# Optimization experiments

Hardware: AMD Instinct MI355X
Metric: run time of the kernel (lower is better)

Reference implementation:

```python
import jax, jax.numpy as jnp
import numpy as np

# Poincare ball with curvature c = 1.0 (geoopt conventions)
C = 1.0
SQC = 1.0  # sqrt(c)
ATANH_EPS = 1e-5
MAXNORM = (1.0 - 4e-3) / SQC  # geoopt float32 projx boundary eps = 4e-3
HD = 256  # hyperbolic_dim


def _norm(x):
    return jnp.clip(jnp.linalg.norm(x, axis=-1, keepdims=True), 1e-15)


def _artanh(x):
    return jnp.arctanh(jnp.clip(x, -1.0 + ATANH_EPS, 1.0 - ATANH_EPS))


def expmap0(u):
    n = _norm(u)
    return jnp.tanh(SQC * n) * u / (SQC * n)


def logmap0(y):
    n = _norm(y)
    return _artanh(SQC * n) * y / (SQC * n)


def projx(x):
    n = _norm(x)
    return jnp.where(n > MAXNORM, x * (MAXNORM / n), x)


def mobius_add(x, y):
    x2 = jnp.sum(x * x, -1, keepdims=True)
    y2 = jnp.sum(y * y, -1, keepdims=True)
    xy = jnp.sum(x * y, -1, keepdims=True)
    num = (1.0 + 2.0 * C * xy + C * y2) * x + (1.0 - C * x2) * y
    den = 1.0 + 2.0 * C * xy + C * C * x2 * y2
    return num / jnp.clip(den, 1e-15)


def mobius_matvec(x, W):
    # geoopt mobius_matvec(weight.T, x) == hyperbolic version of x @ W, W: (in, out)
    xn = _norm(x)
    mx = x @ W
    mxn = _norm(mx)
    return jnp.tanh((mxn / xn) * _artanh(SQC * xn)) * mx / (SQC * mxn)


def mobius_scalar_mul(r, x):
    n = _norm(x)
    return jnp.tanh(r * _artanh(SQC * n)) * x / (SQC * n)


def hlinear(x, W, b):
    # HyperbolicLinear.forward (geoopt manifold ops project by default)
    return projx(mobius_add(projx(mobius_matvec(x, W)), b))


def mobius_tanh(x):
    # MobiusTanh.forward
    return projx(expmap0(jnp.tanh(logmap0(x))))


def zscore(x, eps=1e-8):
    m = jnp.mean(x, axis=1, keepdims=True)
    s = jnp.std(x, axis=1, keepdims=True, ddof=1)  # torch.std is unbiased
    return (x - m) / (s + eps)


def _make_params(key):
    dims_d = [(1711, 1024), (1024, 512), (512, HD)]
    dims_t = [(1711, 1024), (1024, 512), (512, HD)]
    dims_m = [(HD, 64), (64, 32), (32, 2)]
    params = {}
    names = [('Wd', dims_d), ('Wt', dims_t), ('Wm', dims_m)]
    k = key
    for prefix, dims in names:
        for i, (fi, fo) in enumerate(dims, start=1):
            k, k1, k2 = jax.random.split(k, 3)
            params[f'{prefix}{i}'] = jax.random.normal(k1, (fi, fo), dtype=jnp.float32)
            bt = jax.random.normal(k2, (fo,), dtype=jnp.float32) * 0.01
            params[f'b{prefix[1]}{i}'] = expmap0(bt)
    return params


def setup_inputs() -> dict:
    key = jax.random.key(0)
    ks = jax.random.split(key, 8)
    B = 16384
    inp = {
        'drug_chembert': jax.random.normal(ks[0], (B, 768), dtype=jnp.float32),
        'drug_pc': jax.random.normal(ks[1], (B, 11), dtype=jnp.float32),
        'drug_maccs': jax.random.normal(ks[2], (B, 167), dtype=jnp.float32),
        'drug_ecfp': jax.random.normal(ks[3], (B, 765), dtype=jnp.float32),
        'target_esm': jax.random.normal(ks[4], (B, 1280), dtype=jnp.float32),
        'target_pc': jax.random.normal(ks[5], (B, 11), dtype=jnp.float32),
        'target_mer': jax.random.normal(ks[6], (B, 420), dtype=jnp.float32),
    }
    inp.update(_make_params(ks[7]))
    return inp


def reference(drug_chembert, drug_pc, drug_maccs, drug_ecfp,
              target_esm, target_pc, target_mer,
              Wd1, bd1, Wd2, bd2, Wd3, bd3,
              Wt1, bt1, Wt2, bt2, Wt3, bt3,
              Wm1, bm1, Wm2, bm2, Wm3, bm3):
    drug = jnp.concatenate([zscore(drug_chembert), zscore(drug_pc),
                            zscore(drug_maccs), zscore(drug_ecfp)], axis=1)  # [B,1711]
    targ = jnp.concatenate([zscore(target_esm), zscore(target_pc),
                            zscore(target_mer)], axis=1)  # [B,1711]

    h = mobius_tanh(hlinear(expmap0(drug), Wd1, bd1))
    h = mobius_tanh(hlinear(h, Wd2, bd2))
    head = hlinear(h, Wd3, bd3)  # [B,HD]

    t = mobius_tanh(hlinear(expmap0(targ), Wt1, bt1))
    t = mobius_tanh(hlinear(t, Wt2, bt2))
    tail = hlinear(t, Wt3, bt3)  # [B,HD]

    mid = projx(mobius_add(mobius_scalar_mul(0.27, head),
                           mobius_scalar_mul(0.73, tail)))

    r = mobius_tanh(hlinear(mid, Wm1, bm1))
    r = mobius_tanh(hlinear(r, Wm2, bm2))
    return hlinear(r, Wm3, bm3)  # [B,2]
```

## Files before the change

### kernel.cpp

```cpp
#include <hip/hip_runtime.h>
#include <math.h>

#define MAXNORM_F 0.996f

typedef __attribute__((ext_vector_type(8))) short bf16x8;
typedef __attribute__((ext_vector_type(4))) float f32x4;

__device__ __forceinline__ short f2bf(float f) {
    union { float f; unsigned u; } v; v.f = f;
    unsigned r = v.u + 0x7FFF + ((v.u >> 16) & 1);
    return (short)(r >> 16);
}
__device__ __forceinline__ float bf2f(short s) {
    union { unsigned u; float f; } v; v.u = ((unsigned)(unsigned short)s) << 16;
    return v.f;
}

__device__ __forceinline__ float artanh_c(float x) {
    const float lim = 1.0f - 1e-5f;
    x = fminf(fmaxf(x, -lim), lim);
    return 0.5f * logf((1.0f + x) / (1.0f - x));
}

__device__ __forceinline__ float wsum(float v) {
#pragma unroll
    for (int m = 32; m > 0; m >>= 1) v += __shfl_xor(v, m, 64);
    return v;
}

__global__ __launch_bounds__(256) void pack_w_kernel(
    const float* __restrict__ W, int Kreal, int KB, int N, short* __restrict__ out) {
    int e = blockIdx.x * 256 + threadIdx.x;
    int total = (N >> 7) * KB * 2 * 4096;
    if (e >= total) return;
    int j   = e & 7;
    int n   = (e >> 3) & 127;
    int kg  = (e >> 10) & 3;
    int seg = (e >> 12) & 1;
    int rest = e >> 13;
    int kb  = rest % KB;
    int nt  = rest / KB;
    int k = (kb << 5) + (kg << 3) + j;
    int col = (nt << 7) + n;
    float v = (k < Kreal) ? W[(size_t)k * N + col] : 0.f;
    short hi = f2bf(v);
    out[e] = (seg == 0) ? hi : f2bf(v - bf2f(hi));
}

__global__ __launch_bounds__(256) void prep_kernel(
    const float* __restrict__ s0, const float* __restrict__ s1,
    const float* __restrict__ s2, const float* __restrict__ s3,
    int f0, int f1, int f2, int f3,
    short* __restrict__ Xb, float* __restrict__ xn_out) {
    __shared__ float xbuf[4][1712];
    const int lane = threadIdx.x & 63, wave = threadIdx.x >> 6;
    const int row = blockIdx.x * 4 + wave;
    float* xb = xbuf[wave];
    const float* srcs[4] = {s0, s1, s2, s3};
    const int fs[4] = {f0, f1, f2, f3};
    int off = 0;
    for (int b = 0; b < 4; b++) {
        int F = fs[b];
        if (F == 0) break;
        const float* srow = srcs[b] + (size_t)row * F;
        float ps = 0.f;
        for (int i = lane; i < F; i += 64) { float v = srow[i]; xb[off + i] = v; ps += v; }
        float mean = wsum(ps) / (float)F;
        float pq = 0.f;
        for (int i = lane; i < F; i += 64) { float d = xb[off + i] - mean; pq += d * d; }
        float var = wsum(pq) / (float)(F - 1);
        float inv = 1.0f / (sqrtf(var) + 1e-8f);
        for (int i = lane; i < F; i += 64) xb[off + i] = (xb[off + i] - mean) * inv;
        off += F;
    }
    float pn = 0.f;
    for (int i = lane; i < 1711; i += 64) pn += xb[i] * xb[i];
    float n = fmaxf(sqrtf(wsum(pn)), 1e-15f);
    float t = tanhf(n);
    float sc = t / n;
    short* xrow = Xb + (size_t)row * 3456;
    for (int i = lane; i < 1728; i += 64) {
        float v = (i < 1711) ? sc * xb[i] : 0.f;
        short hi = f2bf(v);
        int base = (i >> 5) * 64 + (i & 31);
        xrow[base] = hi;
        xrow[base + 32] = f2bf(v - bf2f(hi));
    }
    if (lane == 0) xn_out[row] = fmaxf(t, 1e-15f);
}

__global__ __launch_bounds__(256) void gemm_mfma(
    const short* __restrict__ A, int lda, int KB,
    const short* __restrict__ Wp,
    float* __restrict__ C, int N, int ntShift) {
    __shared__ short As[2][8192];
    __shared__ short Bs[2][8192];
    const int tid = threadIdx.x;
    const int lane = tid & 63;
    const int wave = __builtin_amdgcn_readfirstlane(tid >> 6);
    const int waveM = wave >> 1, waveN = wave & 1;
    const int kg = lane >> 4, l16 = lane & 15;

    int flat = blockIdx.x;
    int xcd = flat & 7;
    int idx = flat >> 3;
    int q = idx >> ntShift;
    int nt = idx & ((1 << ntShift) - 1);
    int mt = q * 8 + xcd;
    const int m0 = mt * 128;

    f32x4 acc[4][4] = {};
    const short* Bbase = Wp + (size_t)nt * KB * 8192;

    auto stage = [&](int b, int kb) {
#pragma unroll
        for (int c = 0; c < 4; c++) {
            int u = c * 256 + wave * 64 + lane;
            int row = u >> 3;
            int p = (u & 7) ^ (row & 7);
            const short* ga = A + (size_t)(m0 + row) * lda + kb * 64 + p * 8;
            __builtin_amdgcn_global_load_lds(
                (const __attribute__((address_space(1))) unsigned int*)ga,
                (__attribute__((address_space(3))) unsigned int*)&As[b][(c * 256 + wave * 64) * 8],
                16, 0, 0);
        }
#pragma unroll
        for (int c = 0; c < 4; c++) {
            int u = c * 256 + wave * 64 + lane;
            const short* gb = Bbase + (size_t)kb * 8192 + u * 8;
            __builtin_amdgcn_global_load_lds(
                (const __attribute__((address_space(1))) unsigned int*)gb,
                (__attribute__((address_space(3))) unsigned int*)&Bs[b][(c * 256 + wave * 64) * 8],
                16, 0, 0);
        }
    };

    stage(0, 0);
    __syncthreads();
    int cur = 0;
    for (int kb = 0; kb < KB; kb++) {
        if (kb + 1 < KB) stage(cur ^ 1, kb + 1);
        bf16x8 ah[4], al[4], bh[4], bl[4];
#pragma unroll
        for (int mi = 0; mi < 4; mi++) {
            int r = waveM * 64 + mi * 16 + l16;
            int uh = r * 8 + (kg ^ (r & 7));
            int ul = r * 8 + ((4 + kg) ^ (r & 7));
            ah[mi] = *(const bf16x8*)&As[cur][uh * 8];
            al[mi] = *(const bf16x8*)&As[cur][ul * 8];
        }
#pragma unroll
        for (int ni = 0; ni < 4; ni++) {
            int n = waveN * 64 + ni * 16 + l16;
            bh[ni] = *(const bf16x8*)&Bs[cur][(kg * 128 + n) * 8];
            bl[ni] = *(const bf16x8*)&Bs[cur][(512 + kg * 128 + n) * 8];
        }
        __builtin_amdgcn_s_setprio(1);
#pragma unroll
        for (int mi = 0; mi < 4; mi++)
#pragma unroll
            for (int ni = 0; ni < 4; ni++)
                acc[mi][ni] = __builtin_amdgcn_mfma_f32_16x16x32_bf16(ah[mi], bh[ni], acc[mi][ni], 0, 0, 0);
#pragma unroll
        for (int mi = 0; mi < 4; mi++)
#pragma unroll
            for (int ni = 0; ni < 4; ni++)
                acc[mi][ni] = __builtin_amdgcn_mfma_f32_16x16x32_bf16(al[mi], bh[ni], acc[mi][ni], 0, 0, 0);
#pragma unroll
        for (int mi = 0; mi < 4; mi++)
#pragma unroll
            for (int ni = 0; ni < 4; ni++)
                acc[mi][ni] = __builtin_amdgcn_mfma_f32_16x16x32_bf16(ah[mi], bl[ni], acc[mi][ni], 0, 0, 0);
        __builtin_amdgcn_s_setprio(0);
        __syncthreads();
        cur ^= 1;
    }
    const int rbase = m0 + waveM * 64 + (lane >> 4) * 4;
    const int cbase = nt * 128 + waveN * 64 + l16;
#pragma unroll
    for (int mi = 0; mi < 4; mi++)
#pragma unroll
        for (int ni = 0; ni < 4; ni++)
#pragma unroll
            for (int r = 0; r < 4; r++)
                C[(size_t)(rbase + mi * 16 + r) * N + cbase + ni * 16] = acc[mi][ni][r];
}

template<int E>
__device__ float hyper_head_w(float (&v)[E], const float (&bv)[E], float xn, int do_tanh) {
    float p = 0.f;
#pragma unroll
    for (int e = 0; e < E; e++) p += v[e] * v[e];
    float mxn = fmaxf(sqrtf(wsum(p)), 1e-15f);
    float t1 = tanhf((mxn / xn) * artanh_c(xn));
    float ny = fmaxf(t1, 1e-15f);
    float fac = (ny > MAXNORM_F) ? (MAXNORM_F / ny) : 1.0f;
    float sm = t1 * fac / mxn;
    float pa2 = 0.f, pab = 0.f, pb2 = 0.f;
#pragma unroll
    for (int e = 0; e < E; e++) {
        v[e] *= sm;
        pa2 += v[e] * v[e]; pab += v[e] * bv[e]; pb2 += bv[e] * bv[e];
    }
    float a2 = wsum(pa2);
    float ab = wsum(pab);
    float b2 = wsum(pb2);
    float den = fmaxf(1.0f + 2.0f * ab + a2 * b2, 1e-15f);
    float ca = (1.0f + 2.0f * ab + b2) / den;
    float cb = (1.0f - a2) / den;
    float pz2 = 0.f;
#pragma unroll
    for (int e = 0; e < E; e++) {
        v[e] = ca * v[e] + cb * bv[e];
        pz2 += v[e] * v[e];
    }
    float nz = fmaxf(sqrtf(wsum(pz2)), 1e-15f);
    float fz = (nz > MAXNORM_F) ? (MAXNORM_F / nz) : 1.0f;
    float nzp = nz * fz;
    if (!do_tanh) {
#pragma unroll
        for (int e = 0; e < E; e++) v[e] *= fz;
        return nzp;
    }
    float ia = artanh_c(nzp) / nzp * fz;
    float pt2 = 0.f;
#pragma unroll
    for (int e = 0; e < E; e++) {
        v[e] = tanhf(ia * v[e]);
        pt2 += v[e] * v[e];
    }
    float ntn = fmaxf(sqrtf(wsum(pt2)), 1e-15f);
    float to = tanhf(ntn);
    float no = fmaxf(to, 1e-15f);
    float fo = (no > MAXNORM_F) ? (MAXNORM_F / no) : 1.0f;
    float so = to / ntn * fo;
#pragma unroll
    for (int e = 0; e < E; e++) v[e] *= so;
    return fminf(no, MAXNORM_F);
}

template<int VPT>
__global__ __launch_bounds__(256) void epi_kernel(
    const float* __restrict__ MX, int N, const float* __restrict__ bias,
    float* __restrict__ xn_io, short* __restrict__ Xout, int ldx,
    float* __restrict__ Fout, int do_tanh) {
    const int lane = threadIdx.x & 63, wave = threadIdx.x >> 6;
    const int row = blockIdx.x * 4 + wave;
    const float* mrow = MX + (size_t)row * N;
    float v[4 * VPT], bv[4 * VPT];
#pragma unroll
    for (int j = 0; j < VPT; j++) {
        int idx = j * 256 + lane * 4;
        float4 t = *(const float4*)(mrow + idx);
        v[4 * j] = t.x; v[4 * j + 1] = t.y; v[4 * j + 2] = t.z; v[4 * j + 3] = t.w;
        float4 tb = *(const float4*)(bias + idx);
        bv[4 * j] = tb.x; bv[4 * j + 1] = tb.y; bv[4 * j + 2] = tb.z; bv[4 * j + 3] = tb.w;
    }
    float xn = xn_io[row];
    float nrm = hyper_head_w<4 * VPT>(v, bv, xn, do_tanh);
    if (Xout) {
        short* orow = Xout + (size_t)row * ldx;
#pragma unroll
        for (int j = 0; j < VPT; j++) {
            int idx = j * 256 + lane * 4;
            int base = (idx >> 5) * 64 + (idx & 31);
            short4 h4, l4;
            short hi;
            hi = f2bf(v[4 * j + 0]); h4.x = hi; l4.x = f2bf(v[4 * j + 0] - bf2f(hi));
            hi = f2bf(v[4 * j + 1]); h4.y = hi; l4.y = f2bf(v[4 * j + 1] - bf2f(hi));
            hi = f2bf(v[4 * j + 2]); h4.z = hi; l4.z = f2bf(v[4 * j + 2] - bf2f(hi));
            hi = f2bf(v[4 * j + 3]); h4.w = hi; l4.w = f2bf(v[4 * j + 3] - bf2f(hi));
            *(short4*)(orow + base) = h4;
            *(short4*)(orow + base + 32) = l4;
        }
    }
    if (Fout) {
        float* orow = Fout + (size_t)row * N;
#pragma unroll
        for (int j = 0; j < VPT; j++) {
            int idx = j * 256 + lane * 4;
            float4 t;
            t.x = v[4 * j]; t.y = v[4 * j + 1]; t.z = v[4 * j + 2]; t.w = v[4 * j + 3];
            *(float4*)(orow + idx) = t;
        }
    }
    if (lane == 0) xn_io[row] = fmaxf(nrm, 1e-15f);
}

__global__ __launch_bounds__(256) void merge_mlp_kernel(
    const float* __restrict__ head, const float* __restrict__ tail,
    const float* __restrict__ nh_arr, const float* __restrict__ nt_arr,
    const float* __restrict__ Wm1, const float* __restrict__ bm1,
    const float* __restrict__ Wm2, const float* __restrict__ bm2,
    const float* __restrict__ Wm3, const float* __restrict__ bm3,
    float* __restrict__ out) {
    __shared__ float xs[4][256];
    const int lane = threadIdx.x & 63, wave = threadIdx.x >> 6;
    const int row = blockIdx.x * 4 + wave;
    float* x = xs[wave];
    float4 h4 = *(const float4*)(head + (size_t)row * 256 + lane * 4);
    float4 t4 = *(const float4*)(tail + (size_t)row * 256 + lane * 4);
    float A[4] = {h4.x, h4.y, h4.z, h4.w};
    float Bv[4] = {t4.x, t4.y, t4.z, t4.w};
    float nh = nh_arr[row], ntl = nt_arr[row];
    float sh = tanhf(0.27f * artanh_c(nh)) / nh;
    float st = tanhf(0.73f * artanh_c(ntl)) / ntl;
    float px2 = 0.f, py2 = 0.f, pxy = 0.f;
#pragma unroll
    for (int e = 0; e < 4; e++) {
        A[e] *= sh; Bv[e] *= st;
        px2 += A[e] * A[e]; py2 += Bv[e] * Bv[e]; pxy += A[e] * Bv[e];
    }
    float x2 = wsum(px2), y2 = wsum(py2), xy = wsum(pxy);
    float den = fmaxf(1.0f + 2.0f * xy + x2 * y2, 1e-15f);
    float ca = (1.0f + 2.0f * xy + y2) / den, cb = (1.0f - x2) / den;
    float z[4]; float pz2 = 0.f;
#pragma unroll
    for (int e = 0; e < 4; e++) { z[e] = ca * A[e] + cb * Bv[e]; pz2 += z[e] * z[e]; }
    float nz = fmaxf(sqrtf(wsum(pz2)), 1e-15f);
    float fz = (nz > MAXNORM_F) ? (MAXNORM_F / nz) : 1.0f;
    float nmid = nz * fz;
    float4 zs; zs.x = z[0] * fz; zs.y = z[1] * fz; zs.z = z[2] * fz; zs.w = z[3] * fz;
    *(float4*)(x + lane * 4) = zs;

    float v[1], bvv[1];
    {
        float acc = 0.f;
        for (int k = 0; k < 256; k++) acc += x[k] * Wm1[k * 64 + lane];
        v[0] = acc; bvv[0] = bm1[lane];
    }
    float n1 = hyper_head_w<1>(v, bvv, nmid, 1);
    x[lane] = v[0];
    {
        float acc = 0.f;
        if (lane < 32) { for (int k = 0; k < 64; k++) acc += x[k] * Wm2[k * 32 + lane]; }
        v[0] = (lane < 32) ? acc : 0.f;
        bvv[0] = (lane < 32) ? bm2[lane] : 0.f;
    }
    float n2 = hyper_head_w<1>(v, bvv, n1, 1);
    x[lane] = (lane < 32) ? v[0] : 0.f;
    {
        float acc = 0.f;
        if (lane < 2) { for (int k = 0; k < 32; k++) acc += x[k] * Wm3[k * 2 + lane]; }
        v[0] = (lane < 2) ? acc : 0.f;
        bvv[0] = (lane < 2) ? bm3[lane] : 0.f;
    }
    hyper_head_w<1>(v, bvv, n2, 0);
    if (lane < 2) out[(size_t)row * 2 + lane] = v[0];
}

extern "C" void kernel_launch(void* const* d_in, const int* in_sizes, int n_in,
                              void* d_out, int out_size, void* d_ws, size_t ws_size,
                              hipStream_t stream) {
    const float* dch = (const float*)d_in[0];
    const float* dpc = (const float*)d_in[1];
    const float* dmc = (const float*)d_in[2];
    const float* dec = (const float*)d_in[3];
    const float* tes = (const float*)d_in[4];
    const float* tpc = (const float*)d_in[5];
    const float* tme = (const float*)d_in[6];
    const float* Wd1 = (const float*)d_in[7];  const float* bd1 = (const float*)d_in[8];
    const float* Wd2 = (const float*)d_in[9];  const float* bd2 = (const float*)d_in[10];
    const float* Wd3 = (const float*)d_in[11]; const float* bd3 = (const float*)d_in[12];
    const float* Wt1 = (const float*)d_in[13]; const float* bt1 = (const float*)d_in[14];
    const float* Wt2 = (const float*)d_in[15]; const float* bt2 = (const float*)d_in[16];
    const float* Wt3 = (const float*)d_in[17]; const float* bt3 = (const float*)d_in[18];
    const float* Wm1 = (const float*)d_in[19]; const float* bm1 = (const float*)d_in[20];
    const float* Wm2 = (const float*)d_in[21]; const float* bm2 = (const float*)d_in[22];
    const float* Wm3 = (const float*)d_in[23]; const float* bm3 = (const float*)d_in[24];

    const int B = in_sizes[0] / 768;

    float* mx  = (float*)d_ws;
    short* xb  = (short*)(mx + (size_t)B * 1024);
    float* hf_d = (float*)(xb + (size_t)B * 3456);
    float* hf_t = hf_d + (size_t)B * 256;
    float* xn_d = hf_t + (size_t)B * 256;
    float* xn_t = xn_d + B;
    short* wp_d1 = (short*)(xn_t + B);
    short* wp_d2 = wp_d1 + 8 * 54 * 8192;
    short* wp_d3 = wp_d2 + 4 * 32 * 8192;
    short* wp_t1 = wp_d3 + 2 * 16 * 8192;
    short* wp_t2 = wp_t1 + 8 * 54 * 8192;
    short* wp_t3 = wp_t2 + 4 * 32 * 8192;

    dim3 blk(256);
    int e1 = 8 * 54 * 8192, e2 = 4 * 32 * 8192, e3 = 2 * 16 * 8192;
    hipLaunchKernelGGL(pack_w_kernel, dim3((e1 + 255) / 256), blk, 0, stream, Wd1, 1711, 54, 1024, wp_d1);
    hipLaunchKernelGGL(pack_w_kernel, dim3((e2 + 255) / 256), blk, 0, stream, Wd2, 1024, 32, 512, wp_d2);
    hipLaunchKernelGGL(pack_w_kernel, dim3((e3 + 255) / 256), blk, 0, stream, Wd3, 512, 16, 256, wp_d3);
    hipLaunchKernelGGL(pack_w_kernel, dim3((e1 + 255) / 256), blk, 0, stream, Wt1, 1711, 54, 1024, wp_t1);
    hipLaunchKernelGGL(pack_w_kernel, dim3((e2 + 255) / 256), blk, 0, stream, Wt2, 1024, 32, 512, wp_t2);
    hipLaunchKernelGGL(pack_w_kernel, dim3((e3 + 255) / 256), blk, 0, stream, Wt3, 512, 16, 256, wp_t3);

    hipLaunchKernelGGL(prep_kernel, dim3(B / 4), blk, 0, stream,
                       dch, dpc, dmc, dec, 768, 11, 167, 765, xb, xn_d);
    hipLaunchKernelGGL(gemm_mfma, dim3(8 * (B / 128)), blk, 0, stream, xb, 3456, 54, wp_d1, mx, 1024, 3);
    hipLaunchKernelGGL((epi_kernel<4>), dim3(B / 4), blk, 0, stream, mx, 1024, bd1, xn_d, xb, 2048, (float*)nullptr, 1);
    hipLaunchKernelGGL(gemm_mfma, dim3(4 * (B / 128)), blk, 0, stream, xb, 2048, 32, wp_d2, mx, 512, 2);
    hipLaunchKernelGGL((epi_kernel<2>), dim3(B / 4), blk, 0, stream, mx, 512, bd2, xn_d, xb, 1024, (float*)nullptr, 1);
    hipLaunchKernelGGL(gemm_mfma, dim3(2 * (B / 128)), blk, 0, stream, xb, 1024, 16, wp_d3, mx, 256, 1);
    hipLaunchKernelGGL((epi_kernel<1>), dim3(B / 4), blk, 0, stream, mx, 256, bd3, xn_d, (short*)nullptr, 0, hf_d, 0);

    hipLaunchKernelGGL(prep_kernel, dim3(B / 4), blk, 0, stream,
                       tes, tpc, tme, (const float*)nullptr, 1280, 11, 420, 0, xb, xn_t);
    hipLaunchKernelGGL(gemm_mfma, dim3(8 * (B / 128)), blk, 0, stream, xb, 3456, 54, wp_t1, mx, 1024, 3);
    hipLaunchKernelGGL((epi_kernel<4>), dim3(B / 4), blk, 0, stream, mx, 1024, bt1, xn_t, xb, 2048, (float*)nullptr, 1);
    hipLaunchKernelGGL(gemm_mfma, dim3(4 * (B / 128)), blk, 0, stream, xb, 2048, 32, wp_t2, mx, 512, 2);
    hipLaunchKernelGGL((epi_kernel<2>), dim3(B / 4), blk, 0, stream, mx, 512, bt2, xn_t, xb, 1024, (float*)nullptr, 1);
    hipLaunchKernelGGL(gemm_mfma, dim3(2 * (B / 128)), blk, 0, stream, xb, 1024, 16, wp_t3, mx, 256, 1);
    hipLaunchKernelGGL((epi_kernel<1>), dim3(B / 4), blk, 0, stream, mx, 256, bt3, xn_t, (short*)nullptr, 0, hf_t, 0);

    hipLaunchKernelGGL(merge_mlp_kernel, dim3(B / 4), blk, 0, stream,
                       hf_d, hf_t, xn_d, xn_t, Wm1, bm1, Wm2, bm2, Wm3, bm3, (float*)d_out);
}
```

Before: 1.022 ms.

## Load GEMM B tiles directly into registers, bypassing LDS staging

Weight (B) tiles are no longer staged through shared memory; each wave loads its B fragments from global memory straight into registers, using a two-deep register double buffer. The k-loop is unrolled by two so it can alternate between the two register sets while the A tile keeps its LDS double buffer. The aim is to halve LDS usage and LDS read traffic and to raise occupancy. In exchange, waves sharing the same N columns re-read B from L2, and the unroll assumes the number of K blocks is even.

```diff
diff --git a/kernel.cpp b/kernel.cpp
--- a/kernel.cpp
+++ b/kernel.cpp
@@ -94,7 +94,6 @@
     const short* __restrict__ Wp,
     float* __restrict__ C, int N, int ntShift) {
     __shared__ short As[2][8192];
-    __shared__ short Bs[2][8192];
     const int tid = threadIdx.x;
     const int lane = tid & 63;
     const int wave = __builtin_amdgcn_readfirstlane(tid >> 6);
@@ -112,7 +111,7 @@
     f32x4 acc[4][4] = {};
     const short* Bbase = Wp + (size_t)nt * KB * 8192;
 
-    auto stage = [&](int b, int kb) {
+    auto stageA = [&](int b, int kb) {
 #pragma unroll
         for (int c = 0; c < 4; c++) {
             int u = c * 256 + wave * 64 + lane;
@@ -124,36 +123,28 @@
                 (__attribute__((address_space(3))) unsigned int*)&As[b][(c * 256 + wave * 64) * 8],
                 16, 0, 0);
         }
-#pragma unroll
-        for (int c = 0; c < 4; c++) {
-            int u = c * 256 + wave * 64 + lane;
-            const short* gb = Bbase + (size_t)kb * 8192 + u * 8;
-            __builtin_amdgcn_global_load_lds(
-                (const __attribute__((address_space(1))) unsigned int*)gb,
-                (__attribute__((address_space(3))) unsigned int*)&Bs[b][(c * 256 + wave * 64) * 8],
-                16, 0, 0);
-        }
     };
 
-    stage(0, 0);
-    __syncthreads();
-    int cur = 0;
-    for (int kb = 0; kb < KB; kb++) {
-        if (kb + 1 < KB) stage(cur ^ 1, kb + 1);
-        bf16x8 ah[4], al[4], bh[4], bl[4];
+    const int nb = waveN * 64 + l16;
+    auto loadB = [&](int kb, bf16x8 (&bh)[4], bf16x8 (&bl)[4]) {
+        const short* kbase = Bbase + (size_t)kb * 8192;
+#pragma unroll
+        for (int ni = 0; ni < 4; ni++) {
+            int n = nb + ni * 16;
+            bh[ni] = *(const bf16x8*)(kbase + (kg * 128 + n) * 8);
+            bl[ni] = *(const bf16x8*)(kbase + (512 + kg * 128 + n) * 8);
+        }
+    };
+
+    auto compute = [&](int cb, const bf16x8 (&bh)[4], const bf16x8 (&bl)[4]) {
+        bf16x8 ah[4], al[4];
 #pragma unroll
         for (int mi = 0; mi < 4; mi++) {
             int r = waveM * 64 + mi * 16 + l16;
             int uh = r * 8 + (kg ^ (r & 7));
             int ul = r * 8 + ((4 + kg) ^ (r & 7));
-            ah[mi] = *(const bf16x8*)&As[cur][uh * 8];
-            al[mi] = *(const bf16x8*)&As[cur][ul * 8];
-        }
-#pragma unroll
-        for (int ni = 0; ni < 4; ni++) {
-            int n = waveN * 64 + ni * 16 + l16;
-            bh[ni] = *(const bf16x8*)&Bs[cur][(kg * 128 + n) * 8];
-            bl[ni] = *(const bf16x8*)&Bs[cur][(512 + kg * 128 + n) * 8];
+            ah[mi] = *(const bf16x8*)&As[cb][uh * 8];
+            al[mi] = *(const bf16x8*)&As[cb][ul * 8];
         }
         __builtin_amdgcn_s_setprio(1);
 #pragma unroll
@@ -172,6 +163,24 @@
             for (int ni = 0; ni < 4; ni++)
                 acc[mi][ni] = __builtin_amdgcn_mfma_f32_16x16x32_bf16(ah[mi], bl[ni], acc[mi][ni], 0, 0, 0);
         __builtin_amdgcn_s_setprio(0);
+    };
+
+    bf16x8 bh0[4], bl0[4], bh1[4], bl1[4];
+    stageA(0, 0);
+    loadB(0, bh0, bl0);
+    __syncthreads();
+    int cur = 0;
+    for (int t = 0; t < KB; t += 2) {
+        stageA(cur ^ 1, t + 1);
+        loadB(t + 1, bh1, bl1);
+        compute(cur, bh0, bl0);
+        __syncthreads();
+        cur ^= 1;
+        if (t + 2 < KB) {
+            stageA(cur ^ 1, t + 2);
+            loadB(t + 2, bh0, bl0);
+        }
+        compute(cur, bh1, bl1);
         __syncthreads();
         cur ^= 1;
     }
```

Result: slower. 1.075 ms (+5.2%).
